# Optimization experiments

Hardware: AMD Instinct MI355X
Metric: run time of the kernel (lower is better)

Reference implementation:

```python
import jax, jax.numpy as jnp
import numpy as np

DECAY = 0.25  # global `decay` in source
EPS = 1e-5    # nn.BatchNorm2d default eps


def quant(x):
    # MultiSpike1: round(clamp(x, 0, 1))
    return jnp.round(jnp.clip(x, 0.0, 1.0))


def lif(x):
    # mem_update: sequential LIF recurrence over time dim T.
    # step0: mem = x[0] (init mem_old=0, spike=0 reproduces it exactly).
    def step(carry, xi):
        mem_old, spike = carry
        mem = (mem_old - jax.lax.stop_gradient(spike) * 0.5) * DECAY + xi
        s = quant(mem)
        return (mem, s), s

    z = jnp.zeros_like(x[0])
    _, out = jax.lax.scan(step, (z, z), x)
    return out  # [T,B,C,H,W]


def setup_inputs() -> dict:
    key = jax.random.key(0)
    k1, k2 = jax.random.split(key, 2)
    T, B, C1, C2, H, W = 4, 8, 64, 128, 128, 128
    x = jax.random.normal(k1, (T, B, C1, H, W), dtype=jnp.float32)
    # Conv2d(c1=64, c2=128, k=3, s=1, pad=1, bias=False)
    conv_w = jax.random.normal(k2, (C2, C1, 3, 3), dtype=jnp.float32) * 0.05
    gamma = jnp.ones((C2,), dtype=jnp.float32)
    beta = jnp.zeros((C2,), dtype=jnp.float32)
    return {"x": x, "conv_w": conv_w, "gamma": gamma, "beta": beta}


def reference(x, conv_w, gamma, beta):
    T, B, C, H, W = x.shape
    C2 = conv_w.shape[0]
    s = lif(x).reshape(T * B, C, H, W)  # flatten(0,1)
    y = jax.lax.conv_general_dilated(
        s, conv_w, window_strides=(1, 1), padding=((1, 1), (1, 1)),
        dimension_numbers=("NCHW", "OIHW", "NCHW"))
    # BatchNorm2d in training mode: batch statistics over (N,H,W), biased var
    mean = y.mean(axis=(0, 2, 3), keepdims=True)
    var = ((y - mean) ** 2).mean(axis=(0, 2, 3), keepdims=True)
    y = (y - mean) * jax.lax.rsqrt(var + EPS)
    y = y * gamma[None, :, None, None] + beta[None, :, None, None]
    return y.reshape(T, B, C2, H, W)
```

## Files before the change

### kernel.cpp

```cpp
#include <hip/hip_runtime.h>

typedef __bf16 bf16x8 __attribute__((ext_vector_type(8)));
typedef float f32x4 __attribute__((ext_vector_type(4)));

#define TBCHW_PLANE 8388608
#define NPIX 524288.0f
#define NBLK 4096

__global__ __launch_bounds__(256) void prep_w(const float* __restrict__ w,
                                              __bf16* __restrict__ wf) {
    int o = blockIdx.x * 256 + threadIdx.x;
    if (o >= 73728) return;
    int j = o & 7;
    int lane = (o >> 3) & 63;
    int mtile = (o >> 9) & 7;
    int kc = o >> 12;
    int k = kc * 32 + (lane >> 4) * 8 + j;
    int c2 = mtile * 16 + (lane & 15);
    int tap = k >> 6, c = k & 63;
    int kh = tap / 3, kw = tap % 3;
    wf[o] = (__bf16)w[((c2 * 64 + c) * 3 + kh) * 3 + kw];
}

__device__ __forceinline__ float lif_step(float& mem, float sp, float xv) {
    mem = (mem - sp * 0.5f) * 0.25f + xv;
    return rintf(fminf(fmaxf(mem, 0.0f), 1.0f));
}

__global__ __launch_bounds__(256) void lif_kernel(const float* __restrict__ x,
                                                  __bf16* __restrict__ s) {
    __shared__ __bf16 lds[2 * 128 * 72];
    int b = blockIdx.x >> 7, h = blockIdx.x & 127;
    int tid = threadIdx.x;

    float4 mem[8], sp[8];
#pragma unroll
    for (int i = 0; i < 8; ++i) { mem[i] = make_float4(0,0,0,0); sp[i] = make_float4(0,0,0,0); }

    for (int half = 0; half < 2; ++half) {
        if (half) __syncthreads();
#pragma unroll
        for (int t2 = 0; t2 < 2; ++t2) {
            int t = half * 2 + t2;
#pragma unroll
            for (int i = 0; i < 8; ++i) {
                int p = tid + 256 * i;
                int c = p >> 5, w0 = (p & 31) * 4;
                const float4 xv = *(const float4*)(x + (size_t)t * TBCHW_PLANE +
                                   (((size_t)b * 64 + c) * 128 + h) * 128 + w0);
                float s0 = lif_step(mem[i].x, sp[i].x, xv.x);
                float s1 = lif_step(mem[i].y, sp[i].y, xv.y);
                float s2 = lif_step(mem[i].z, sp[i].z, xv.z);
                float s3 = lif_step(mem[i].w, sp[i].w, xv.w);
                sp[i] = make_float4(s0, s1, s2, s3);
                __bf16* dst = &lds[(t2 * 128 + w0) * 72 + c];
                dst[0] = (__bf16)s0; dst[72] = (__bf16)s1;
                dst[144] = (__bf16)s2; dst[216] = (__bf16)s3;
            }
        }
        __syncthreads();
#pragma unroll
        for (int i = 0; i < 8; ++i) {
            int u = tid + 256 * i;
            int t2 = u >> 10, inner = u & 1023;
            int w = inner >> 3, c8 = inner & 7;
            bf16x8 v = *(const bf16x8*)&lds[(t2 * 128 + w) * 72 + c8 * 8];
            int n = (half * 2 + t2) * 8 + b;
            *(bf16x8*)(s + (((size_t)n * 128 + h) * 128 + w) * 64 + c8 * 8) = v;
        }
    }
}

__global__ __launch_bounds__(256) void conv_kernel(const __bf16* __restrict__ s,
                                                   const __bf16* __restrict__ wf,
                                                   float* __restrict__ out,
                                                   float* __restrict__ part) {
    __shared__ __align__(16) __bf16 sb[3 * 130 * 72];
    int n = blockIdx.x >> 7, h = blockIdx.x & 127;
    int tid = threadIdx.x;

#pragma unroll
    for (int i = 0; i < 12; ++i) {
        int u = tid + 256 * i;
        int row = u >> 10;
        int inner = u & 1023;
        int hh = h + row - 1;
        int w = inner >> 3, c8 = inner & 7;
        bf16x8 v;
        if (hh >= 0 && hh < 128) {
            v = *(const bf16x8*)(s + (((size_t)n * 128 + hh) * 128) * 64 + inner * 8);
        } else {
#pragma unroll
            for (int z = 0; z < 8; ++z) v[z] = (__bf16)0.0f;
        }
        *(bf16x8*)&sb[(row * 130 + (w + 1)) * 72 + c8 * 8] = v;
    }
    if (tid < 48) {
        int row = tid / 16, q16 = tid % 16;
        int wl = (q16 & 1) ? 129 : 0, c8 = q16 >> 1;
        bf16x8 z;
#pragma unroll
        for (int e = 0; e < 8; ++e) z[e] = (__bf16)0.0f;
        *(bf16x8*)&sb[(row * 130 + wl) * 72 + c8 * 8] = z;
    }
    __syncthreads();

    int lane = tid & 63, wave = tid >> 6;
    int wm = wave >> 1, wn = wave & 1;
    int lm = lane & 15, q = lane >> 4;

    f32x4 acc[4][4];
#pragma unroll
    for (int i = 0; i < 4; ++i)
#pragma unroll
        for (int j = 0; j < 4; ++j)
#pragma unroll
            for (int e = 0; e < 4; ++e) acc[i][j][e] = 0.0f;

#pragma unroll
    for (int kc = 0; kc < 18; ++kc) {
        int tap = kc >> 1;
        int kh = tap / 3, kw = tap % 3;
        int cb = (kc & 1) * 32;
        bf16x8 a[4], bb[4];
#pragma unroll
        for (int i = 0; i < 4; ++i)
            a[i] = *(const bf16x8*)(wf + (((size_t)kc * 8 + wm * 4 + i) * 64 + lane) * 8);
#pragma unroll
        for (int j = 0; j < 4; ++j) {
            int wl = wn * 64 + j * 16 + lm + kw;
            bb[j] = *(const bf16x8*)&sb[(kh * 130 + wl) * 72 + cb + q * 8];
        }
#pragma unroll
        for (int i = 0; i < 4; ++i)
#pragma unroll
            for (int j = 0; j < 4; ++j)
                acc[i][j] = __builtin_amdgcn_mfma_f32_16x16x32_bf16(a[i], bb[j], acc[i][j], 0, 0, 0);
    }

    __syncthreads();
    float2* P = (float2*)sb;

#pragma unroll
    for (int i = 0; i < 4; ++i) {
#pragma unroll
        for (int r = 0; r < 4; ++r) {
            int c2 = wm * 64 + i * 16 + q * 4 + r;
            size_t ob = ((size_t)(n * 128 + c2) * 128 + h) * 128 + wn * 64 + lm;
            float sum = 0.0f, ssq = 0.0f;
#pragma unroll
            for (int j = 0; j < 4; ++j) {
                float v = acc[i][j][r];
                out[ob + j * 16] = v;
                sum += v; ssq += v * v;
            }
#pragma unroll
            for (int d = 8; d > 0; d >>= 1) {
                sum += __shfl_down(sum, d);
                ssq += __shfl_down(ssq, d);
            }
            if (lm == 0) {
                P[wave * 64 + i * 16 + q * 4 + r] = make_float2(sum, ssq);
            }
        }
    }
    __syncthreads();
    {
        int stat = tid >> 7, c2x = tid & 127;
        int wp = c2x >> 6, idx = c2x & 63;
        float2 a2 = P[(wp * 2) * 64 + idx];
        float2 b2 = P[(wp * 2 + 1) * 64 + idx];
        float val = stat ? (a2.y + b2.y) : (a2.x + b2.x);
        part[(size_t)tid * NBLK + blockIdx.x] = val;
    }
}

__global__ __launch_bounds__(256) void reduce_stats(const float* __restrict__ part,
                                                    const float* __restrict__ gamma,
                                                    const float* __restrict__ beta,
                                                    float* __restrict__ ss) {
    int c = blockIdx.x;
    int tid = threadIdx.x;
    const float* ps = part + (size_t)c * NBLK;
    const float* pq = part + (size_t)(128 + c) * NBLK;
    float sum = 0.0f, ssq = 0.0f;
    for (int i = tid; i < NBLK; i += 256) { sum += ps[i]; ssq += pq[i]; }
#pragma unroll
    for (int d = 32; d > 0; d >>= 1) {
        sum += __shfl_down(sum, d);
        ssq += __shfl_down(ssq, d);
    }
    __shared__ float2 wred[4];
    if ((tid & 63) == 0) wred[tid >> 6] = make_float2(sum, ssq);
    __syncthreads();
    if (tid == 0) {
        float S = 0.0f, Q = 0.0f;
#pragma unroll
        for (int w2 = 0; w2 < 4; ++w2) { S += wred[w2].x; Q += wred[w2].y; }
        const float inv = 1.0f / NPIX;
        float mean = S * inv;
        float var = Q * inv - mean * mean;
        float sc = gamma[c] * rsqrtf(var + 1e-5f);
        ss[c] = sc;
        ss[128 + c] = beta[c] - mean * sc;
    }
}

__global__ __launch_bounds__(256) void bn_apply(float* __restrict__ out,
                                                const float* __restrict__ ss) {
    size_t i4 = (size_t)blockIdx.x * 256 + threadIdx.x;
    int c2 = (int)((i4 >> 12) & 127);
    float sc = ss[c2], sh = ss[128 + c2];
    float4* p = (float4*)out + i4;
    float4 v = *p;
    v.x = v.x * sc + sh; v.y = v.y * sc + sh;
    v.z = v.z * sc + sh; v.w = v.w * sc + sh;
    *p = v;
}

extern "C" void kernel_launch(void* const* d_in, const int* in_sizes, int n_in,
                              void* d_out, int out_size, void* d_ws, size_t ws_size,
                              hipStream_t stream) {
    const float* x     = (const float*)d_in[0];
    const float* cw    = (const float*)d_in[1];
    const float* gamma = (const float*)d_in[2];
    const float* beta  = (const float*)d_in[3];
    float* out = (float*)d_out;

    char* ws = (char*)d_ws;
    __bf16* s     = (__bf16*)ws;
    __bf16* wfrag = (__bf16*)(ws + 67108864);
    float*  part  = (float*)(ws + 67108864 + 147456);
    float*  ss    = part + 256 * NBLK;

    prep_w      <<<288,   256, 0, stream>>>(cw, wfrag);
    lif_kernel  <<<1024,  256, 0, stream>>>(x, s);
    conv_kernel <<<NBLK,  256, 0, stream>>>(s, wfrag, out, part);
    reduce_stats<<<128,   256, 0, stream>>>(part, gamma, beta, ss);
    bn_apply    <<<65536, 256, 0, stream>>>(out, ss);
}
```

Baseline: 584.5 us.

## Make conv blocks persistent over 8 rows with an LDS ring buffer and async global-to-LDS loads

Each conv block now handles eight output rows instead of one. Input rows stream through a 4-slot LDS ring using global_load_lds, so each row is staged once and reused across three output rows rather than reloaded three times. The LDS layout uses an XOR swizzle in place of padding to avoid bank conflicts, and the first three weight fragments are kept in registers. In exchange the grid shrinks to 512 blocks, which lowers parallelism, and correctness depends on the ring-slot synchronisation.

Result: slower. 641.1 us (+9.7%).

```diff
diff --git a/kernel.cpp b/kernel.cpp
--- a/kernel.cpp
+++ b/kernel.cpp
@@ -6,6 +6,7 @@
 #define TBCHW_PLANE 8388608
 #define NPIX 524288.0f
 #define NBLK 4096
+#define SLOT_B 16640
 
 __global__ __launch_bounds__(256) void prep_w(const float* __restrict__ w,
                                               __bf16* __restrict__ wf) {
@@ -71,107 +72,134 @@
     }
 }
 
-__global__ __launch_bounds__(256) void conv_kernel(const __bf16* __restrict__ s,
-                                                   const __bf16* __restrict__ wf,
-                                                   float* __restrict__ out,
-                                                   float* __restrict__ part) {
-    __shared__ __align__(16) __bf16 sb[3 * 130 * 72];
-    int n = blockIdx.x >> 7, h = blockIdx.x & 127;
-    int tid = threadIdx.x;
-
-#pragma unroll
-    for (int i = 0; i < 12; ++i) {
-        int u = tid + 256 * i;
-        int row = u >> 10;
-        int inner = u & 1023;
-        int hh = h + row - 1;
-        int w = inner >> 3, c8 = inner & 7;
-        bf16x8 v;
-        if (hh >= 0 && hh < 128) {
-            v = *(const bf16x8*)(s + (((size_t)n * 128 + hh) * 128) * 64 + inner * 8);
-        } else {
-#pragma unroll
-            for (int z = 0; z < 8; ++z) v[z] = (__bf16)0.0f;
-        }
-        *(bf16x8*)&sb[(row * 130 + (w + 1)) * 72 + c8 * 8] = v;
-    }
-    if (tid < 48) {
-        int row = tid / 16, q16 = tid % 16;
-        int wl = (q16 & 1) ? 129 : 0, c8 = q16 >> 1;
-        bf16x8 z;
-#pragma unroll
-        for (int e = 0; e < 8; ++e) z[e] = (__bf16)0.0f;
-        *(bf16x8*)&sb[(row * 130 + wl) * 72 + c8 * 8] = z;
-    }
+__device__ __forceinline__ void stage_row(const __bf16* __restrict__ s, int n, int hh,
+                                          char* slot, int tid) {
+    if (hh >= 0 && hh < 128) {
+        const char* src = (const char*)s + (((size_t)n * 128 + hh) << 14);
+#pragma unroll
+        for (int i = 0; i < 4; ++i) {
+            int g = i * 256 + tid;
+            int w = g >> 3;
+            int sg = (w << 7) + (((g & 7) ^ ((w + 1) & 7)) << 4);
+            __builtin_amdgcn_global_load_lds(
+                (const __attribute__((address_space(1))) unsigned int*)(src + sg),
+                (__attribute__((address_space(3))) unsigned int*)(slot + 128 + g * 16),
+                16, 0, 0);
+        }
+    } else {
+        f32x4 z = {0.f, 0.f, 0.f, 0.f};
+#pragma unroll
+        for (int i = 0; i < 4; ++i) {
+            int g = i * 256 + tid;
+            *(f32x4*)(slot + 128 + g * 16) = z;
+        }
+    }
+}
+
+__global__ __launch_bounds__(256, 2) void conv_kernel(const __bf16* __restrict__ s,
+                                                      const __bf16* __restrict__ wf,
+                                                      float* __restrict__ out,
+                                                      float* __restrict__ part) {
+    __shared__ __align__(16) char ring[4 * SLOT_B];
+    __shared__ float2 P[2][256];
+    const int n  = blockIdx.x >> 4;
+    const int h0 = (blockIdx.x & 15) << 3;
+    const int tid = threadIdx.x;
+    const int lane = tid & 63, wave = tid >> 6;
+    const int wm = wave >> 1, wn = wave & 1;
+    const int lm = lane & 15, q = lane >> 4;
+
+    if (tid < 64) {
+        int slot = tid >> 4, col = (tid >> 3) & 1, g8 = tid & 7;
+        f32x4 z = {0.f, 0.f, 0.f, 0.f};
+        *(f32x4*)(ring + slot * SLOT_B + (col ? 129 * 128 : 0) + g8 * 16) = z;
+    }
+
+    bf16x8 ar0[4], ar1[4], ar2[4];
+#pragma unroll
+    for (int i = 0; i < 4; ++i) {
+        ar0[i] = *(const bf16x8*)(wf + (((size_t)0 * 8 + wm * 4 + i) * 64 + lane) * 8);
+        ar1[i] = *(const bf16x8*)(wf + (((size_t)1 * 8 + wm * 4 + i) * 64 + lane) * 8);
+        ar2[i] = *(const bf16x8*)(wf + (((size_t)2 * 8 + wm * 4 + i) * 64 + lane) * 8);
+    }
+
+    stage_row(s, n, h0 - 1, ring + ((h0 + 3) & 3) * SLOT_B, tid);
+    stage_row(s, n, h0,     ring + ((h0 + 0) & 3) * SLOT_B, tid);
+    stage_row(s, n, h0 + 1, ring + ((h0 + 1) & 3) * SLOT_B, tid);
     __syncthreads();
 
-    int lane = tid & 63, wave = tid >> 6;
-    int wm = wave >> 1, wn = wave & 1;
-    int lm = lane & 15, q = lane >> 4;
-
-    f32x4 acc[4][4];
-#pragma unroll
-    for (int i = 0; i < 4; ++i)
-#pragma unroll
-        for (int j = 0; j < 4; ++j)
-#pragma unroll
-            for (int e = 0; e < 4; ++e) acc[i][j][e] = 0.0f;
-
-#pragma unroll
-    for (int kc = 0; kc < 18; ++kc) {
-        int tap = kc >> 1;
-        int kh = tap / 3, kw = tap % 3;
-        int cb = (kc & 1) * 32;
-        bf16x8 a[4], bb[4];
+    const int wbyte = (wn * 64 + lm) * 128;
+
+#pragma unroll 1
+    for (int hs = 0; hs < 8; ++hs) {
+        const int h = h0 + hs;
+        if (hs < 7) stage_row(s, n, h + 2, ring + ((h + 2) & 3) * SLOT_B, tid);
+
+        const char* rb0 = ring + ((h + 3) & 3) * SLOT_B;
+        const char* rb1 = ring + ((h + 0) & 3) * SLOT_B;
+        const char* rb2 = ring + ((h + 1) & 3) * SLOT_B;
+
+        f32x4 acc[4][4];
 #pragma unroll
         for (int i = 0; i < 4; ++i)
-            a[i] = *(const bf16x8*)(wf + (((size_t)kc * 8 + wm * 4 + i) * 64 + lane) * 8);
-#pragma unroll
-        for (int j = 0; j < 4; ++j) {
-            int wl = wn * 64 + j * 16 + lm + kw;
-            bb[j] = *(const bf16x8*)&sb[(kh * 130 + wl) * 72 + cb + q * 8];
-        }
-#pragma unroll
-        for (int i = 0; i < 4; ++i)
 #pragma unroll
             for (int j = 0; j < 4; ++j)
-                acc[i][j] = __builtin_amdgcn_mfma_f32_16x16x32_bf16(a[i], bb[j], acc[i][j], 0, 0, 0);
-    }
-
-    __syncthreads();
-    float2* P = (float2*)sb;
-
-#pragma unroll
-    for (int i = 0; i < 4; ++i) {
-#pragma unroll
-        for (int r = 0; r < 4; ++r) {
-            int c2 = wm * 64 + i * 16 + q * 4 + r;
-            size_t ob = ((size_t)(n * 128 + c2) * 128 + h) * 128 + wn * 64 + lm;
-            float sum = 0.0f, ssq = 0.0f;
-#pragma unroll
-            for (int j = 0; j < 4; ++j) {
-                float v = acc[i][j][r];
-                out[ob + j * 16] = v;
-                sum += v; ssq += v * v;
+#pragma unroll
+                for (int e = 0; e < 4; ++e) acc[i][j][e] = 0.0f;
+
+#pragma unroll
+        for (int kc = 0; kc < 18; ++kc) {
+            const int tap = kc >> 1;
+            const int kh = tap / 3, kw = tap - kh * 3;
+            const int c8b = (kc & 1) * 4;
+            const char* rb = (kh == 0) ? rb0 : (kh == 1) ? rb1 : rb2;
+            const int off = kw * 128 + ((((c8b + q) ^ ((lm + kw) & 7))) << 4);
+            bf16x8 av[4], bv[4];
+#pragma unroll
+            for (int i = 0; i < 4; ++i)
+                av[i] = (kc == 0) ? ar0[i] : (kc == 1) ? ar1[i] : (kc == 2) ? ar2[i]
+                      : *(const bf16x8*)(wf + (((size_t)kc * 8 + wm * 4 + i) * 64 + lane) * 8);
+#pragma unroll
+            for (int j = 0; j < 4; ++j)
+                bv[j] = *(const bf16x8*)(rb + wbyte + j * 2048 + off);
+#pragma unroll
+            for (int i = 0; i < 4; ++i)
+#pragma unroll
+                for (int j = 0; j < 4; ++j)
+                    acc[i][j] = __builtin_amdgcn_mfma_f32_16x16x32_bf16(av[i], bv[j], acc[i][j], 0, 0, 0);
+        }
+
+#pragma unroll
+        for (int i = 0; i < 4; ++i) {
+#pragma unroll
+            for (int r = 0; r < 4; ++r) {
+                int c2 = wm * 64 + i * 16 + q * 4 + r;
+                size_t ob = ((size_t)(n * 128 + c2) * 128 + h) * 128 + wn * 64 + lm;
+                float sum = 0.0f, ssq = 0.0f;
+#pragma unroll
+                for (int j = 0; j < 4; ++j) {
+                    float v = acc[i][j][r];
+                    out[ob + j * 16] = v;
+                    sum += v; ssq += v * v;
+                }
+#pragma unroll
+                for (int d = 8; d > 0; d >>= 1) {
+                    sum += __shfl_down(sum, d);
+                    ssq += __shfl_down(ssq, d);
+                }
+                if (lm == 0)
+                    P[hs & 1][wave * 64 + i * 16 + q * 4 + r] = make_float2(sum, ssq);
             }
-#pragma unroll
-            for (int d = 8; d > 0; d >>= 1) {
-                sum += __shfl_down(sum, d);
-                ssq += __shfl_down(ssq, d);
-            }
-            if (lm == 0) {
-                P[wave * 64 + i * 16 + q * 4 + r] = make_float2(sum, ssq);
-            }
-        }
-    }
-    __syncthreads();
-    {
-        int stat = tid >> 7, c2x = tid & 127;
-        int wp = c2x >> 6, idx = c2x & 63;
-        float2 a2 = P[(wp * 2) * 64 + idx];
-        float2 b2 = P[(wp * 2 + 1) * 64 + idx];
-        float val = stat ? (a2.y + b2.y) : (a2.x + b2.x);
-        part[(size_t)tid * NBLK + blockIdx.x] = val;
+        }
+        __syncthreads();
+        {
+            int stat = tid >> 7, c2x = tid & 127;
+            int wp = c2x >> 6, idx = c2x & 63;
+            float2 a2 = P[hs & 1][(wp * 2) * 64 + idx];
+            float2 b2 = P[hs & 1][(wp * 2 + 1) * 64 + idx];
+            float val = stat ? (a2.y + b2.y) : (a2.x + b2.x);
+            part[(size_t)tid * NBLK + (blockIdx.x << 3) + hs] = val;
+        }
     }
 }
 
@@ -235,7 +263,7 @@
 
     prep_w      <<<288,   256, 0, stream>>>(cw, wfrag);
     lif_kernel  <<<1024,  256, 0, stream>>>(x, s);
-    conv_kernel <<<NBLK,  256, 0, stream>>>(s, wfrag, out, part);
+    conv_kernel <<<512,   256, 0, stream>>>(s, wfrag, out, part);
     reduce_stats<<<128,   256, 0, stream>>>(part, gamma, beta, ss);
     bn_apply    <<<65536, 256, 0, stream>>>(out, ss);
 }
```
